# Kernel tuning notes

Hardware: AMD Instinct MI355X
Metric: run time of the kernel (lower is better)

## Reference

```python
import jax, jax.numpy as jnp
import numpy as np

D_MODEL = 1024
NUM_HEADS = 16
DEPTH = D_MODEL // NUM_HEADS
B, S = 2, 2048


def setup_inputs() -> dict:
    key = jax.random.key(0)
    ks = jax.random.split(key, 12)
    scale = 1.0 / np.sqrt(D_MODEL)
    inp = {
        "Q": jax.random.normal(ks[0], (B, S, D_MODEL), jnp.float32),
        "K": jax.random.normal(ks[1], (B, S, D_MODEL), jnp.float32),
        "V": jax.random.normal(ks[2], (B, S, D_MODEL), jnp.float32),
        # causal mask: 1 where attention is disallowed (strictly upper triangular)
        "mask": jnp.triu(jnp.ones((1, 1, S, S), jnp.float32), k=1),
        "Wq": jax.random.normal(ks[3], (D_MODEL, D_MODEL), jnp.float32) * scale,
        "bq": jnp.zeros((D_MODEL,), jnp.float32),
        "Wk": jax.random.normal(ks[4], (D_MODEL, D_MODEL), jnp.float32) * scale,
        "bk": jnp.zeros((D_MODEL,), jnp.float32),
        "Wv": jax.random.normal(ks[5], (D_MODEL, D_MODEL), jnp.float32) * scale,
        "bv": jnp.zeros((D_MODEL,), jnp.float32),
        "Wo": jax.random.normal(ks[6], (D_MODEL, D_MODEL), jnp.float32) * scale,
        "bo": jnp.zeros((D_MODEL,), jnp.float32),
    }
    return inp


def _split_heads(x):
    # [B, S, d_model] -> [B, H, S, depth]
    b, s, _ = x.shape
    return x.reshape(b, s, NUM_HEADS, DEPTH).transpose(0, 2, 1, 3)


def reference(Q, K, V, mask, Wq, bq, Wk, bk, Wv, bv, Wo, bo):
    q = _split_heads(Q @ Wq + bq)  # [B,H,S,depth]
    k = _split_heads(K @ Wk + bk)
    v = _split_heads(V @ Wv + bv)

    scale = 1.0 / jnp.sqrt(jnp.asarray(DEPTH, q.dtype))
    scores = jnp.einsum("bhqd,bhkd->bhqk", q, k) * scale
    scores = scores + mask * (-1e9)
    attn = jax.nn.softmax(scores, axis=-1)  # [B,H,S,S]
    ctx = jnp.einsum("bhqk,bhkd->bhqd", attn, v)

    # combine heads: [B,H,S,depth] -> [B,S,d_model]
    ctx = ctx.transpose(0, 2, 1, 3).reshape(Q.shape[0], -1, D_MODEL)
    out = ctx @ Wo + bo
    return out, attn
```

## Files before the change

### kernel.cpp

```cpp
#include <hip/hip_runtime.h>
#include <hip/hip_bf16.h>
#include <cstdint>
#include <cstddef>


typedef __bf16 bf16x8 __attribute__((ext_vector_type(8)));
typedef float  f32x4  __attribute__((ext_vector_type(4)));
typedef unsigned short u16;
typedef unsigned int   u32;

using gas_p = const __attribute__((address_space(1))) void*;
using las_p = __attribute__((address_space(3))) void*;

static __device__ __forceinline__ u16 f2bf(float x) {
    unsigned u = __builtin_bit_cast(unsigned, x);
    u += 0x7FFFu + ((u >> 16) & 1u);
    return (u16)(u >> 16);
}
static __device__ __forceinline__ u32 pk2(float a, float b) {
    return (u32)f2bf(a) | ((u32)f2bf(b) << 16);
}
static __device__ __forceinline__ f32x4 mfma16(bf16x8 a, bf16x8 b, f32x4 c) {
    return __builtin_amdgcn_mfma_f32_16x16x32_bf16(a, b, c, 0, 0, 0);
}
static __device__ __forceinline__ bf16x8 ldb8(const u16* p) {
    return *reinterpret_cast<const bf16x8*>(p);
}

__global__ __launch_bounds__(256) void transpose_cvt_k(const float* __restrict__ Wq,
                                                       const float* __restrict__ Wk,
                                                       const float* __restrict__ Wv,
                                                       const float* __restrict__ Wo,
                                                       u16* __restrict__ Wt3,
                                                       u16* __restrict__ Wto) {
    const int z = blockIdx.z;
    const float* in = (z == 0) ? Wq : (z == 1) ? Wk : (z == 2) ? Wv : Wo;
    u16* out = (z < 3) ? (Wt3 + (size_t)z * 1048576) : Wto;
    __shared__ float t[32][33];
    const int tx = threadIdx.x, ty = threadIdx.y;
    const int x  = blockIdx.x * 32 + tx;
    const int y0 = blockIdx.y * 32 + ty;
#pragma unroll
    for (int j = 0; j < 32; j += 8)
        t[ty + j][tx] = in[(size_t)(y0 + j) * 1024 + x];
    __syncthreads();
    const int x2 = blockIdx.y * 32 + tx;
    const int y2 = blockIdx.x * 32 + ty;
#pragma unroll
    for (int j = 0; j < 32; j += 8)
        out[(size_t)(y2 + j) * 1024 + x2] = f2bf(t[tx][ty + j]);
}

__global__ __launch_bounds__(256) void gemm_qkv_k(const float* __restrict__ Qf,
                                                  const float* __restrict__ Kf,
                                                  const float* __restrict__ Vf,
                                                  const u16* __restrict__ Wt3,
                                                  const float* __restrict__ bq,
                                                  const float* __restrict__ bk,
                                                  const float* __restrict__ bv,
                                                  u16* __restrict__ qf,
                                                  u16* __restrict__ kf,
                                                  u16* __restrict__ vtf,
                                                  float* __restrict__ attn) {
    constexpr int Kd = 1024;
    constexpr int S = 2048;
    const int z = blockIdx.z;

    if (z == 3) {
        float* attn_h = attn + (size_t)blockIdx.y * S * S;
        const int bx = blockIdx.x;
        const int ro = threadIdx.x >> 4, cc = threadIdx.x & 15;
        const f32x4 zz = {0.f, 0.f, 0.f, 0.f};
        for (int c = 1; c < 32; ++c) {
            float* base = attn_h + (size_t)(bx * 8 * c) * S + c * 64 + cc * 4;
            const int nrows = 8 * c;
            for (int i = ro; i < nrows; i += 16)
                __builtin_nontemporal_store(zz, reinterpret_cast<f32x4*>(base + (size_t)i * S));
        }
        return;
    }

    const float* Af = (z == 0) ? Qf : (z == 1) ? Kf : Vf;
    const u16* Bt = Wt3 + (size_t)z * 1048576;
    const float* bias = (z == 0) ? bq : (z == 1) ? bk : bv;

    __shared__ __align__(16) u16 As[128 * 64];
    __shared__ __align__(16) u16 Bs[128 * 64];
    const int tid = threadIdx.x;
    const int w = tid >> 6, lane = tid & 63;
    const int g = lane >> 4, lr = lane & 15;
    const int wr = w >> 1, wc = w & 1;
    const int bm = blockIdx.y * 128, bn = blockIdx.x * 128;

    f32x4 acc[4][4];
#pragma unroll
    for (int a = 0; a < 4; ++a)
#pragma unroll
        for (int b = 0; b < 4; ++b) acc[a][b] = f32x4{0.f, 0.f, 0.f, 0.f};

    const int arow = tid >> 3;
    const int ach  = tid & 7;

    for (int kt = 0; kt < Kd; kt += 64) {
        float4 av[8];
#pragma unroll
        for (int it = 0; it < 4; ++it) {
            const float* src = Af + (size_t)(bm + it * 32 + arow) * Kd + kt + ach * 8;
            av[it * 2]     = *reinterpret_cast<const float4*>(src);
            av[it * 2 + 1] = *reinterpret_cast<const float4*>(src + 4);
        }
#pragma unroll
        for (int it = 0; it < 4; ++it) {
            const int t2  = it * 256 + tid;
            const int row = t2 >> 3, ch = t2 & 7;
            const int ub  = (it * 256 + w * 64) * 8;
            __builtin_amdgcn_global_load_lds(
                (gas_p)(Bt + (size_t)(bn + row) * Kd + kt + ch * 8),
                (las_p)(Bs + ub), 16, 0, 0);
        }
        asm volatile("s_waitcnt vmcnt(0)" ::: "memory");
#pragma unroll
        for (int it = 0; it < 4; ++it) {
            uint4 pk;
            pk.x = pk2(av[it * 2].x, av[it * 2].y);
            pk.y = pk2(av[it * 2].z, av[it * 2].w);
            pk.z = pk2(av[it * 2 + 1].x, av[it * 2 + 1].y);
            pk.w = pk2(av[it * 2 + 1].z, av[it * 2 + 1].w);
            *reinterpret_cast<uint4*>(As + (it * 32 + arow) * 64 + ach * 8) = pk;
        }
        __syncthreads();
#pragma unroll
        for (int kk = 0; kk < 2; ++kk) {
            bf16x8 af[4], bfv[4];
#pragma unroll
            for (int mi = 0; mi < 4; ++mi)
                af[mi] = ldb8(As + (wr * 64 + mi * 16 + lr) * 64 + kk * 32 + g * 8);
#pragma unroll
            for (int ni = 0; ni < 4; ++ni)
                bfv[ni] = ldb8(Bs + (wc * 64 + ni * 16 + lr) * 64 + kk * 32 + g * 8);
#pragma unroll
            for (int mi = 0; mi < 4; ++mi)
#pragma unroll
                for (int ni = 0; ni < 4; ++ni)
                    acc[mi][ni] = mfma16(af[mi], bfv[ni], acc[mi][ni]);
        }
        __syncthreads();
    }

#pragma unroll
    for (int ni = 0; ni < 4; ++ni) {
        const int col = bn + wc * 64 + ni * 16 + lr;
        const float bvv = bias[col];
#pragma unroll
        for (int mi = 0; mi < 4; ++mi) {
            const int row0 = bm + wr * 64 + mi * 16 + g * 4;
            f32x4 c = acc[mi][ni];
            if (z == 2) {
                const int b = row0 >> 11, s0 = row0 & 2047;
                const int h = col >> 6,  d = col & 63;
                ushort4 pk;
                pk.x = f2bf(c[0] + bvv); pk.y = f2bf(c[1] + bvv);
                pk.z = f2bf(c[2] + bvv); pk.w = f2bf(c[3] + bvv);
                *reinterpret_cast<ushort4*>(
                    vtf + ((size_t)(b * 16 + h) * 64 + d) * 2048 + s0) = pk;
            } else {
#pragma unroll
                for (int i = 0; i < 4; ++i) {
                    const int row = row0 + i;
                    const int b = row >> 11, s = row & 2047;
                    const int h = col >> 6,  d = col & 63;
                    u16* dst = (z == 0) ? qf : kf;
                    dst[((size_t)(b * 16 + h) * 2048 + s) * 64 + d] =
                        f2bf(c[i] + bvv);
                }
            }
        }
    }
}

__global__ __launch_bounds__(256) void gemm_out_k(const u16* __restrict__ A,
                                                  const u16* __restrict__ Bt,
                                                  const float* __restrict__ bias,
                                                  float* __restrict__ dst) {
    constexpr int Kd = 1024;
    __shared__ __align__(16) u16 As[128 * 64];
    __shared__ __align__(16) u16 Bs[128 * 64];
    const int tid = threadIdx.x;
    const int w = tid >> 6, lane = tid & 63;
    const int g = lane >> 4, lr = lane & 15;
    const int wr = w >> 1, wc = w & 1;
    const int bm = blockIdx.y * 128, bn = blockIdx.x * 128;

    f32x4 acc[4][4];
#pragma unroll
    for (int a = 0; a < 4; ++a)
#pragma unroll
        for (int b = 0; b < 4; ++b) acc[a][b] = f32x4{0.f, 0.f, 0.f, 0.f};

    for (int kt = 0; kt < Kd; kt += 64) {
#pragma unroll
        for (int it = 0; it < 4; ++it) {
            const int t2  = it * 256 + tid;
            const int row = t2 >> 3, ch = t2 & 7;
            const int ub  = (it * 256 + w * 64) * 8;
            __builtin_amdgcn_global_load_lds(
                (gas_p)(A + (size_t)(bm + row) * Kd + kt + ch * 8),
                (las_p)(As + ub), 16, 0, 0);
            __builtin_amdgcn_global_load_lds(
                (gas_p)(Bt + (size_t)(bn + row) * Kd + kt + ch * 8),
                (las_p)(Bs + ub), 16, 0, 0);
        }
        __syncthreads();
#pragma unroll
        for (int kk = 0; kk < 2; ++kk) {
            bf16x8 af[4], bfv[4];
#pragma unroll
            for (int mi = 0; mi < 4; ++mi)
                af[mi] = ldb8(As + (wr * 64 + mi * 16 + lr) * 64 + kk * 32 + g * 8);
#pragma unroll
            for (int ni = 0; ni < 4; ++ni)
                bfv[ni] = ldb8(Bs + (wc * 64 + ni * 16 + lr) * 64 + kk * 32 + g * 8);
#pragma unroll
            for (int mi = 0; mi < 4; ++mi)
#pragma unroll
                for (int ni = 0; ni < 4; ++ni)
                    acc[mi][ni] = mfma16(af[mi], bfv[ni], acc[mi][ni]);
        }
        __syncthreads();
    }

#pragma unroll
    for (int ni = 0; ni < 4; ++ni) {
        const int col = bn + wc * 64 + ni * 16 + lr;
        const float bvv = bias[col];
#pragma unroll
        for (int mi = 0; mi < 4; ++mi) {
            const int row0 = bm + wr * 64 + mi * 16 + g * 4;
            f32x4 c = acc[mi][ni];
#pragma unroll
            for (int i = 0; i < 4; ++i)
                __builtin_nontemporal_store(c[i] + bvv,
                                            dst + (size_t)(row0 + i) * 1024 + col);
        }
    }
}

__global__ __launch_bounds__(256) void attn_fused_k(const u16* __restrict__ qbuf,
                                                    const u16* __restrict__ kbuf,
                                                    const u16* __restrict__ vtbuf,
                                                    float* __restrict__ attn,
                                                    u16* __restrict__ ctx) {
    constexpr int S = 2048;
    constexpr float SC2 = 0.125f * 1.44269504088896340736f;
    const int bh = blockIdx.y;
    const int pr = blockIdx.x;
    const int tid = threadIdx.x;
    const int w = tid >> 6, lane = tid & 63, g = lane >> 4, lr = lane & 15;

    const u16* qh = qbuf + (size_t)bh * S * 64;
    const u16* kh = kbuf + (size_t)bh * S * 64;
    const u16* vh = vtbuf + (size_t)bh * 64 * S;
    float* attn_h = attn + (size_t)bh * S * S;

    __shared__ __align__(16) u16 Ks[3][64 * 64];
    __shared__ __align__(16) u16 Vs[3][64 * 64];
    __shared__ __align__(16) u16 P[4][16][72];

    const int srow8 = lane >> 3;
    const int scol  = ((lane & 7) ^ srow8) * 8;
    const int swq   = (lr & 7) << 3;
    const int b = bh >> 4, h = bh & 15;

    for (int phase = 0; phase < 2; ++phase) {
        const int j  = phase ? (31 - pr) : pr;
        const int nT = j + 1;
        const int qb = j * 64 + w * 16;
        const int qrow = qb + lr;

        const u16* qp = qh + (size_t)qrow * 64;
        const bf16x8 q0 = ldb8(qp + g * 8);
        const bf16x8 q1 = ldb8(qp + 32 + g * 8);

        const int i0 = w * 2, i1 = w * 2 + 1;
        const int r0 = i0 * 8 + srow8, r1 = i1 * 8 + srow8;

        float m2 = -1e30f, l = 0.f;
        __builtin_amdgcn_global_load_lds((gas_p)(kh + (size_t)r0 * 64 + scol),
                                         (las_p)(Ks[0] + i0 * 512), 16, 0, 0);
        __builtin_amdgcn_global_load_lds((gas_p)(kh + (size_t)r1 * 64 + scol),
                                         (las_p)(Ks[0] + i1 * 512), 16, 0, 0);
        if (nT > 1) {
            __builtin_amdgcn_global_load_lds((gas_p)(kh + (size_t)(64 + r0) * 64 + scol),
                                             (las_p)(Ks[1] + i0 * 512), 16, 0, 0);
            __builtin_amdgcn_global_load_lds((gas_p)(kh + (size_t)(64 + r1) * 64 + scol),
                                             (las_p)(Ks[1] + i1 * 512), 16, 0, 0);
            asm volatile("s_waitcnt vmcnt(2)" ::: "memory");
        } else {
            asm volatile("s_waitcnt vmcnt(0)" ::: "memory");
        }
        __builtin_amdgcn_s_barrier();
        __builtin_amdgcn_sched_barrier(0);

        int cur = 0, stg = 2;
        for (int t = 0; t < nT; ++t) {
            if (t + 2 < nT) {
                const int kr0 = (t + 2) * 64;
                __builtin_amdgcn_global_load_lds(
                    (gas_p)(kh + (size_t)(kr0 + r0) * 64 + scol),
                    (las_p)(Ks[stg] + i0 * 512), 16, 0, 0);
                __builtin_amdgcn_global_load_lds(
                    (gas_p)(kh + (size_t)(kr0 + r1) * 64 + scol),
                    (las_p)(Ks[stg] + i1 * 512), 16, 0, 0);
                __builtin_amdgcn_sched_barrier(0);
            }
            const int kc = t * 64;
            f32x4 c[4];
#pragma unroll
            for (int n = 0; n < 4; ++n) {
                const u16* kr = Ks[cur] + (n * 16 + lr) * 64;
                f32x4 z4 = {0.f, 0.f, 0.f, 0.f};
                z4   = mfma16(ldb8(kr + ((g * 8) ^ swq)), q0, z4);
                c[n] = mfma16(ldb8(kr + ((32 + g * 8) ^ swq)), q1, z4);
            }
            float xm = -__builtin_inff();
#pragma unroll
            for (int n = 0; n < 4; ++n)
#pragma unroll
                for (int i = 0; i < 4; ++i) {
                    const int kcol = kc + n * 16 + g * 4 + i;
                    const float v = (kcol <= qrow) ? c[n][i] * SC2 : -__builtin_inff();
                    c[n][i] = v;
                    xm = fmaxf(xm, v);
                }
            xm = fmaxf(xm, __shfl_xor(xm, 16));
            xm = fmaxf(xm, __shfl_xor(xm, 32));
            const float mn = fmaxf(m2, xm);
            float sum = 0.f;
#pragma unroll
            for (int n = 0; n < 4; ++n)
#pragma unroll
                for (int i = 0; i < 4; ++i) sum += exp2f(c[n][i] - mn);
            sum += __shfl_xor(sum, 16);
            sum += __shfl_xor(sum, 32);
            l = l * exp2f(m2 - mn) + sum;
            m2 = mn;
            if (t + 1 < nT) {
                if (t + 2 < nT) {
                    asm volatile("s_waitcnt vmcnt(2)" ::: "memory");
                } else {
                    asm volatile("s_waitcnt vmcnt(0)" ::: "memory");
                }
                __builtin_amdgcn_s_barrier();
                __builtin_amdgcn_sched_barrier(0);
            }
            cur = (cur == 2) ? 0 : cur + 1;
            stg = (stg == 2) ? 0 : stg + 1;
        }
        const float invl = 1.f / l;

        f32x4 acc[4];
#pragma unroll
        for (int dn = 0; dn < 4; ++dn) acc[dn] = f32x4{0.f, 0.f, 0.f, 0.f};

        __syncthreads();
        __builtin_amdgcn_global_load_lds((gas_p)(kh + (size_t)r0 * 64 + scol),
                                         (las_p)(Ks[0] + i0 * 512), 16, 0, 0);
        __builtin_amdgcn_global_load_lds((gas_p)(kh + (size_t)r1 * 64 + scol),
                                         (las_p)(Ks[0] + i1 * 512), 16, 0, 0);
        __builtin_amdgcn_global_load_lds((gas_p)(vh + (size_t)r0 * 2048 + scol),
                                         (las_p)(Vs[0] + i0 * 512), 16, 0, 0);
        __builtin_amdgcn_global_load_lds((gas_p)(vh + (size_t)r1 * 2048 + scol),
                                         (las_p)(Vs[0] + i1 * 512), 16, 0, 0);
        if (nT > 1) {
            __builtin_amdgcn_global_load_lds((gas_p)(kh + (size_t)(64 + r0) * 64 + scol),
                                             (las_p)(Ks[1] + i0 * 512), 16, 0, 0);
            __builtin_amdgcn_global_load_lds((gas_p)(kh + (size_t)(64 + r1) * 64 + scol),
                                             (las_p)(Ks[1] + i1 * 512), 16, 0, 0);
            __builtin_amdgcn_global_load_lds((gas_p)(vh + (size_t)r0 * 2048 + 64 + scol),
                                             (las_p)(Vs[1] + i0 * 512), 16, 0, 0);
            __builtin_amdgcn_global_load_lds((gas_p)(vh + (size_t)r1 * 2048 + 64 + scol),
                                             (las_p)(Vs[1] + i1 * 512), 16, 0, 0);
            asm volatile("s_waitcnt vmcnt(4)" ::: "memory");
        } else {
            asm volatile("s_waitcnt vmcnt(0)" ::: "memory");
        }
        __builtin_amdgcn_s_barrier();
        __builtin_amdgcn_sched_barrier(0);

        cur = 0; stg = 2;
        for (int t = 0; t < nT; ++t) {
            if (t + 2 < nT) {
                const int kr0 = (t + 2) * 64;
                __builtin_amdgcn_global_load_lds(
                    (gas_p)(kh + (size_t)(kr0 + r0) * 64 + scol),
                    (las_p)(Ks[stg] + i0 * 512), 16, 0, 0);
                __builtin_amdgcn_global_load_lds(
                    (gas_p)(kh + (size_t)(kr0 + r1) * 64 + scol),
                    (las_p)(Ks[stg] + i1 * 512), 16, 0, 0);
                __builtin_amdgcn_global_load_lds(
                    (gas_p)(vh + (size_t)r0 * 2048 + kr0 + scol),
                    (las_p)(Vs[stg] + i0 * 512), 16, 0, 0);
                __builtin_amdgcn_global_load_lds(
                    (gas_p)(vh + (size_t)r1 * 2048 + kr0 + scol),
                    (las_p)(Vs[stg] + i1 * 512), 16, 0, 0);
                __builtin_amdgcn_sched_barrier(0);
            }
            const int kc = t * 64;
            f32x4 c[4];
#pragma unroll
            for (int n = 0; n < 4; ++n) {
                const u16* kr = Ks[cur] + (n * 16 + lr) * 64;
                f32x4 z4 = {0.f, 0.f, 0.f, 0.f};
                z4   = mfma16(ldb8(kr + ((g * 8) ^ swq)), q0, z4);
                c[n] = mfma16(ldb8(kr + ((32 + g * 8) ^ swq)), q1, z4);
            }
#pragma unroll
            for (int n = 0; n < 4; ++n) {
                f32x4 pv;
#pragma unroll
                for (int i = 0; i < 4; ++i) {
                    const int kcol = kc + n * 16 + g * 4 + i;
                    pv[i] = (kcol <= qrow) ? exp2f(c[n][i] * SC2 - m2) * invl : 0.f;
                }
                __builtin_nontemporal_store(
                    pv, reinterpret_cast<f32x4*>(attn_h + (size_t)qrow * S + kc + n * 16 + g * 4));
                uint2 pr2;
                pr2.x = pk2(pv[0], pv[1]);
                pr2.y = pk2(pv[2], pv[3]);
                *reinterpret_cast<uint2*>(&P[w][lr][n * 16 + g * 4]) = pr2;
            }
            asm volatile("s_waitcnt lgkmcnt(0)" ::: "memory");
            __builtin_amdgcn_sched_barrier(0);
#pragma unroll
            for (int kk = 0; kk < 2; ++kk) {
                const bf16x8 pa = ldb8(&P[w][lr][kk * 32 + g * 8]);
#pragma unroll
                for (int dn = 0; dn < 4; ++dn) {
                    const u16* vr = Vs[cur] + (dn * 16 + lr) * 64;
                    acc[dn] = mfma16(pa, ldb8(vr + ((kk * 32 + g * 8) ^ swq)), acc[dn]);
                }
            }
            if (t + 1 < nT) {
                if (t + 2 < nT) {
                    asm volatile("s_waitcnt vmcnt(8)" ::: "memory");
                } else {
                    asm volatile("s_waitcnt vmcnt(4)" ::: "memory");
                }
                __builtin_amdgcn_s_barrier();
                __builtin_amdgcn_sched_barrier(0);
            }
            cur = (cur == 2) ? 0 : cur + 1;
            stg = (stg == 2) ? 0 : stg + 1;
        }

#pragma unroll
        for (int dn = 0; dn < 4; ++dn)
#pragma unroll
            for (int i = 0; i < 4; ++i) {
                const size_t row = (size_t)b * S + qb + g * 4 + i;
                ctx[row * 1024 + h * 64 + dn * 16 + lr] = f2bf(acc[dn][i]);
            }
        __syncthreads();
    }
}

extern "C" void kernel_launch(void* const* d_in, const int* in_sizes, int n_in,
                              void* d_out, int out_size, void* d_ws, size_t ws_size,
                              hipStream_t stream) {
    (void)in_sizes; (void)n_in; (void)out_size; (void)ws_size;

    const float* Q  = (const float*)d_in[0];
    const float* K  = (const float*)d_in[1];
    const float* V  = (const float*)d_in[2];
    const float* Wq = (const float*)d_in[4];
    const float* bq = (const float*)d_in[5];
    const float* Wk = (const float*)d_in[6];
    const float* bk = (const float*)d_in[7];
    const float* Wv = (const float*)d_in[8];
    const float* bv = (const float*)d_in[9];
    const float* Wo = (const float*)d_in[10];
    const float* bo = (const float*)d_in[11];

    char* ws = (char*)d_ws;
    u16* Wt3 = (u16*)(ws);
    u16* Wto = (u16*)(ws + ((size_t)6  << 20));
    u16* qf  = (u16*)(ws + ((size_t)8  << 20));
    u16* kf  = (u16*)(ws + ((size_t)16 << 20));
    u16* vtf = (u16*)(ws + ((size_t)24 << 20));
    u16* ctx = (u16*)(ws + ((size_t)32 << 20));

    float* out  = (float*)d_out;
    float* attn = out + (size_t)4096 * 1024;

    transpose_cvt_k<<<dim3(32, 32, 4), dim3(32, 8), 0, stream>>>(Wq, Wk, Wv, Wo, Wt3, Wto);

    gemm_qkv_k<<<dim3(8, 32, 4), 256, 0, stream>>>(Q, K, V, Wt3, bq, bk, bv,
                                                   qf, kf, vtf, attn);

    attn_fused_k<<<dim3(16, 32), 256, 0, stream>>>(qf, kf, vtf, attn, ctx);

    gemm_out_k<<<dim3(8, 32), 256, 0, stream>>>(ctx, Wto, bo, out);
}
```

Baseline: 321.6 us.

## Split fused attention into stats and PV kernels, move zero-fill into stats pass

Splits the two-pass fused attention kernel into a stats kernel that computes the per-row max and log-sum and writes the masked-zero region of attn, and a separate PV kernel that recomputes scores, writes normalized probabilities and accumulates the context. The attn zero-fill moves out of the QKV GEMM launch, the K/V pipelines drop from triple to double buffering, and nontemporal stores become plain stores. This cuts LDS use and removes the extra z-slice from the GEMM, at the cost of an additional launch and shallower prefetch that may expose more load latency.

Result: slower. 332.0 us (+3.2%).

```diff
diff --git a/kernel.cpp b/kernel.cpp
--- a/kernel.cpp
+++ b/kernel.cpp
@@ -60,26 +60,9 @@
                                                   const float* __restrict__ bv,
                                                   u16* __restrict__ qf,
                                                   u16* __restrict__ kf,
-                                                  u16* __restrict__ vtf,
-                                                  float* __restrict__ attn) {
+                                                  u16* __restrict__ vtf) {
     constexpr int Kd = 1024;
-    constexpr int S = 2048;
     const int z = blockIdx.z;
-
-    if (z == 3) {
-        float* attn_h = attn + (size_t)blockIdx.y * S * S;
-        const int bx = blockIdx.x;
-        const int ro = threadIdx.x >> 4, cc = threadIdx.x & 15;
-        const f32x4 zz = {0.f, 0.f, 0.f, 0.f};
-        for (int c = 1; c < 32; ++c) {
-            float* base = attn_h + (size_t)(bx * 8 * c) * S + c * 64 + cc * 4;
-            const int nrows = 8 * c;
-            for (int i = ro; i < nrows; i += 16)
-                __builtin_nontemporal_store(zz, reinterpret_cast<f32x4*>(base + (size_t)i * S));
-        }
-        return;
-    }
-
     const float* Af = (z == 0) ? Qf : (z == 1) ? Kf : Vf;
     const u16* Bt = Wt3 + (size_t)z * 1048576;
     const float* bias = (z == 0) ? bq : (z == 1) ? bk : bv;
@@ -239,17 +222,15 @@
             f32x4 c = acc[mi][ni];
 #pragma unroll
             for (int i = 0; i < 4; ++i)
-                __builtin_nontemporal_store(c[i] + bvv,
-                                            dst + (size_t)(row0 + i) * 1024 + col);
-        }
-    }
-}
-
-__global__ __launch_bounds__(256) void attn_fused_k(const u16* __restrict__ qbuf,
+                dst[(size_t)(row0 + i) * 1024 + col] = c[i] + bvv;
+        }
+    }
+}
+
+__global__ __launch_bounds__(256) void attn_stats_k(const u16* __restrict__ qbuf,
                                                     const u16* __restrict__ kbuf,
-                                                    const u16* __restrict__ vtbuf,
-                                                    float* __restrict__ attn,
-                                                    u16* __restrict__ ctx) {
+                                                    float* __restrict__ ml,
+                                                    float* __restrict__ attn) {
     constexpr int S = 2048;
     constexpr float SC2 = 0.125f * 1.44269504088896340736f;
     const int bh = blockIdx.y;
@@ -259,17 +240,15 @@
 
     const u16* qh = qbuf + (size_t)bh * S * 64;
     const u16* kh = kbuf + (size_t)bh * S * 64;
-    const u16* vh = vtbuf + (size_t)bh * 64 * S;
     float* attn_h = attn + (size_t)bh * S * S;
 
-    __shared__ __align__(16) u16 Ks[3][64 * 64];
-    __shared__ __align__(16) u16 Vs[3][64 * 64];
-    __shared__ __align__(16) u16 P[4][16][72];
+    __shared__ __align__(16) u16 Ks[2][64 * 64];
 
     const int srow8 = lane >> 3;
     const int scol  = ((lane & 7) ^ srow8) * 8;
     const int swq   = (lr & 7) << 3;
-    const int b = bh >> 4, h = bh & 15;
+    const int i0 = w * 2, i1 = w * 2 + 1;
+    const int r0 = i0 * 8 + srow8, r1 = i1 * 8 + srow8;
 
     for (int phase = 0; phase < 2; ++phase) {
         const int j  = phase ? (31 - pr) : pr;
@@ -281,36 +260,22 @@
         const bf16x8 q0 = ldb8(qp + g * 8);
         const bf16x8 q1 = ldb8(qp + 32 + g * 8);
 
-        const int i0 = w * 2, i1 = w * 2 + 1;
-        const int r0 = i0 * 8 + srow8, r1 = i1 * 8 + srow8;
-
         float m2 = -1e30f, l = 0.f;
         __builtin_amdgcn_global_load_lds((gas_p)(kh + (size_t)r0 * 64 + scol),
                                          (las_p)(Ks[0] + i0 * 512), 16, 0, 0);
         __builtin_amdgcn_global_load_lds((gas_p)(kh + (size_t)r1 * 64 + scol),
                                          (las_p)(Ks[0] + i1 * 512), 16, 0, 0);
-        if (nT > 1) {
-            __builtin_amdgcn_global_load_lds((gas_p)(kh + (size_t)(64 + r0) * 64 + scol),
-                                             (las_p)(Ks[1] + i0 * 512), 16, 0, 0);
-            __builtin_amdgcn_global_load_lds((gas_p)(kh + (size_t)(64 + r1) * 64 + scol),
-                                             (las_p)(Ks[1] + i1 * 512), 16, 0, 0);
-            asm volatile("s_waitcnt vmcnt(2)" ::: "memory");
-        } else {
-            asm volatile("s_waitcnt vmcnt(0)" ::: "memory");
-        }
-        __builtin_amdgcn_s_barrier();
-        __builtin_amdgcn_sched_barrier(0);
-
-        int cur = 0, stg = 2;
+        __syncthreads();
         for (int t = 0; t < nT; ++t) {
-            if (t + 2 < nT) {
-                const int kr0 = (t + 2) * 64;
+            const int cur = t & 1;
+            if (t + 1 < nT) {
+                const int kr0 = (t + 1) * 64;
                 __builtin_amdgcn_global_load_lds(
                     (gas_p)(kh + (size_t)(kr0 + r0) * 64 + scol),
-                    (las_p)(Ks[stg] + i0 * 512), 16, 0, 0);
+                    (las_p)(Ks[cur ^ 1] + i0 * 512), 16, 0, 0);
                 __builtin_amdgcn_global_load_lds(
                     (gas_p)(kh + (size_t)(kr0 + r1) * 64 + scol),
-                    (las_p)(Ks[stg] + i1 * 512), 16, 0, 0);
+                    (las_p)(Ks[cur ^ 1] + i1 * 512), 16, 0, 0);
                 __builtin_amdgcn_sched_barrier(0);
             }
             const int kc = t * 64;
@@ -345,24 +310,66 @@
             l = l * exp2f(m2 - mn) + sum;
             m2 = mn;
             if (t + 1 < nT) {
-                if (t + 2 < nT) {
-                    asm volatile("s_waitcnt vmcnt(2)" ::: "memory");
-                } else {
-                    asm volatile("s_waitcnt vmcnt(0)" ::: "memory");
-                }
+                asm volatile("s_waitcnt vmcnt(0)" ::: "memory");
                 __builtin_amdgcn_s_barrier();
                 __builtin_amdgcn_sched_barrier(0);
             }
-            cur = (cur == 2) ? 0 : cur + 1;
-            stg = (stg == 2) ? 0 : stg + 1;
-        }
-        const float invl = 1.f / l;
+        }
+        if (g == 0) ml[(size_t)bh * S + qrow] = m2 + __log2f(l);
+
+        const int z0 = nT * 64;
+        const f32x4 zz = {0.f, 0.f, 0.f, 0.f};
+        float* rowp = attn_h + (size_t)qrow * S;
+        for (int c0 = z0 + g * 4; c0 < S; c0 += 16)
+            *reinterpret_cast<f32x4*>(rowp + c0) = zz;
+        __syncthreads();
+    }
+}
+
+__global__ __launch_bounds__(256) void attn_pv_k(const u16* __restrict__ qbuf,
+                                                 const u16* __restrict__ kbuf,
+                                                 const u16* __restrict__ vtbuf,
+                                                 const float* __restrict__ ml,
+                                                 float* __restrict__ attn,
+                                                 u16* __restrict__ ctx) {
+    constexpr int S = 2048;
+    constexpr float SC2 = 0.125f * 1.44269504088896340736f;
+    const int bh = blockIdx.y;
+    const int pr = blockIdx.x;
+    const int tid = threadIdx.x;
+    const int w = tid >> 6, lane = tid & 63, g = lane >> 4, lr = lane & 15;
+
+    const u16* qh = qbuf + (size_t)bh * S * 64;
+    const u16* kh = kbuf + (size_t)bh * S * 64;
+    const u16* vh = vtbuf + (size_t)bh * 64 * S;
+    float* attn_h = attn + (size_t)bh * S * S;
+
+    __shared__ __align__(16) u16 Ks[2][64 * 64];
+    __shared__ __align__(16) u16 Vs[2][64 * 64];
+    __shared__ __align__(16) u16 P[4][16][72];
+
+    const int srow8 = lane >> 3;
+    const int scol  = ((lane & 7) ^ srow8) * 8;
+    const int swq   = (lr & 7) << 3;
+    const int i0 = w * 2, i1 = w * 2 + 1;
+    const int r0 = i0 * 8 + srow8, r1 = i1 * 8 + srow8;
+    const int b = bh >> 4, h = bh & 15;
+
+    for (int phase = 0; phase < 2; ++phase) {
+        const int j  = phase ? (31 - pr) : pr;
+        const int nT = j + 1;
+        const int qb = j * 64 + w * 16;
+        const int qrow = qb + lr;
+
+        const u16* qp = qh + (size_t)qrow * 64;
+        const bf16x8 q0 = ldb8(qp + g * 8);
+        const bf16x8 q1 = ldb8(qp + 32 + g * 8);
+        const float mfin = ml[(size_t)bh * S + qrow];
 
         f32x4 acc[4];
 #pragma unroll
         for (int dn = 0; dn < 4; ++dn) acc[dn] = f32x4{0.f, 0.f, 0.f, 0.f};
 
-        __syncthreads();
         __builtin_amdgcn_global_load_lds((gas_p)(kh + (size_t)r0 * 64 + scol),
                                          (las_p)(Ks[0] + i0 * 512), 16, 0, 0);
         __builtin_amdgcn_global_load_lds((gas_p)(kh + (size_t)r1 * 64 + scol),
@@ -371,38 +378,24 @@
                                          (las_p)(Vs[0] + i0 * 512), 16, 0, 0);
         __builtin_amdgcn_global_load_lds((gas_p)(vh + (size_t)r1 * 2048 + scol),
                                          (las_p)(Vs[0] + i1 * 512), 16, 0, 0);
-        if (nT > 1) {
-            __builtin_amdgcn_global_load_lds((gas_p)(kh + (size_t)(64 + r0) * 64 + scol),
-                                             (las_p)(Ks[1] + i0 * 512), 16, 0, 0);
-            __builtin_amdgcn_global_load_lds((gas_p)(kh + (size_t)(64 + r1) * 64 + scol),
-                                             (las_p)(Ks[1] + i1 * 512), 16, 0, 0);
-            __builtin_amdgcn_global_load_lds((gas_p)(vh + (size_t)r0 * 2048 + 64 + scol),
-                                             (las_p)(Vs[1] + i0 * 512), 16, 0, 0);
-            __builtin_amdgcn_global_load_lds((gas_p)(vh + (size_t)r1 * 2048 + 64 + scol),
-                                             (las_p)(Vs[1] + i1 * 512), 16, 0, 0);
-            asm volatile("s_waitcnt vmcnt(4)" ::: "memory");
-        } else {
-            asm volatile("s_waitcnt vmcnt(0)" ::: "memory");
-        }
-        __builtin_amdgcn_s_barrier();
-        __builtin_amdgcn_sched_barrier(0);
-
-        cur = 0; stg = 2;
+        __syncthreads();
+
         for (int t = 0; t < nT; ++t) {
-            if (t + 2 < nT) {
-                const int kr0 = (t + 2) * 64;
+            const int cur = t & 1;
+            if (t + 1 < nT) {
+                const int kr0 = (t + 1) * 64;
                 __builtin_amdgcn_global_load_lds(
                     (gas_p)(kh + (size_t)(kr0 + r0) * 64 + scol),
-                    (las_p)(Ks[stg] + i0 * 512), 16, 0, 0);
+                    (las_p)(Ks[cur ^ 1] + i0 * 512), 16, 0, 0);
                 __builtin_amdgcn_global_load_lds(
                     (gas_p)(kh + (size_t)(kr0 + r1) * 64 + scol),
-                    (las_p)(Ks[stg] + i1 * 512), 16, 0, 0);
+                    (las_p)(Ks[cur ^ 1] + i1 * 512), 16, 0, 0);
                 __builtin_amdgcn_global_load_lds(
                     (gas_p)(vh + (size_t)r0 * 2048 + kr0 + scol),
-                    (las_p)(Vs[stg] + i0 * 512), 16, 0, 0);
+                    (las_p)(Vs[cur ^ 1] + i0 * 512), 16, 0, 0);
                 __builtin_amdgcn_global_load_lds(
                     (gas_p)(vh + (size_t)r1 * 2048 + kr0 + scol),
-                    (las_p)(Vs[stg] + i1 * 512), 16, 0, 0);
+                    (las_p)(Vs[cur ^ 1] + i1 * 512), 16, 0, 0);
                 __builtin_amdgcn_sched_barrier(0);
             }
             const int kc = t * 64;
@@ -420,10 +413,10 @@
 #pragma unroll
                 for (int i = 0; i < 4; ++i) {
                     const int kcol = kc + n * 16 + g * 4 + i;
-                    pv[i] = (kcol <= qrow) ? exp2f(c[n][i] * SC2 - m2) * invl : 0.f;
+                    pv[i] = (kcol <= qrow) ? exp2f(c[n][i] * SC2 - mfin) : 0.f;
                 }
-                __builtin_nontemporal_store(
-                    pv, reinterpret_cast<f32x4*>(attn_h + (size_t)qrow * S + kc + n * 16 + g * 4));
+                *reinterpret_cast<f32x4*>(
+                    attn_h + (size_t)qrow * S + kc + n * 16 + g * 4) = pv;
                 uint2 pr2;
                 pr2.x = pk2(pv[0], pv[1]);
                 pr2.y = pk2(pv[2], pv[3]);
@@ -441,16 +434,10 @@
                 }
             }
             if (t + 1 < nT) {
-                if (t + 2 < nT) {
-                    asm volatile("s_waitcnt vmcnt(8)" ::: "memory");
-                } else {
-                    asm volatile("s_waitcnt vmcnt(4)" ::: "memory");
-                }
+                asm volatile("s_waitcnt vmcnt(4)" ::: "memory");
                 __builtin_amdgcn_s_barrier();
                 __builtin_amdgcn_sched_barrier(0);
             }
-            cur = (cur == 2) ? 0 : cur + 1;
-            stg = (stg == 2) ? 0 : stg + 1;
         }
 
 #pragma unroll
@@ -488,16 +475,19 @@
     u16* kf  = (u16*)(ws + ((size_t)16 << 20));
     u16* vtf = (u16*)(ws + ((size_t)24 << 20));
     u16* ctx = (u16*)(ws + ((size_t)32 << 20));
+    float* ml = (float*)(ws + ((size_t)40 << 20));
 
     float* out  = (float*)d_out;
     float* attn = out + (size_t)4096 * 1024;
 
     transpose_cvt_k<<<dim3(32, 32, 4), dim3(32, 8), 0, stream>>>(Wq, Wk, Wv, Wo, Wt3, Wto);
 
-    gemm_qkv_k<<<dim3(8, 32, 4), 256, 0, stream>>>(Q, K, V, Wt3, bq, bk, bv,
-                                                   qf, kf, vtf, attn);
-
-    attn_fused_k<<<dim3(16, 32), 256, 0, stream>>>(qf, kf, vtf, attn, ctx);
+    gemm_qkv_k<<<dim3(8, 32, 3), 256, 0, stream>>>(Q, K, V, Wt3, bq, bk, bv,
+                                                   qf, kf, vtf);
+
+    attn_stats_k<<<dim3(16, 32), 256, 0, stream>>>(qf, kf, ml, attn);
+
+    attn_pv_k<<<dim3(16, 32), 256, 0, stream>>>(qf, kf, vtf, ml, attn, ctx);
 
     gemm_out_k<<<dim3(8, 32), 256, 0, stream>>>(ctx, Wto, bo, out);
 }
```
